# Performance work log

Hardware: AMD Instinct MI355X
Metric: run time of the kernel (lower is better)

## Reference

```python
import jax, jax.numpy as jnp
import numpy as np

B, S, DIM = 2, 1024, 4096
H, QLORA, KVLORA = 32, 1536, 512
NOPE, ROPE, VD = 128, 64, 128
QK_HEAD = NOPE + ROPE
SCALE = QK_HEAD ** -0.5
EPS = 1e-6
NEG = -1e9


def rms_norm(x, w):
    xf = x.astype(jnp.float32)
    y = xf * jax.lax.rsqrt(jnp.mean(xf * xf, axis=-1, keepdims=True) + EPS)
    return (y * w).astype(x.dtype)


def apply_rope(x, fc):
    # x: [b, s, h, r] with interleaved complex pairs; fc: [s, r//2, 2] = (cos, sin)
    b, s, h, r = x.shape
    xr = x.reshape(b, s, h, r // 2, 2)
    xe, xo = xr[..., 0], xr[..., 1]
    cos = fc[None, :, None, :, 0]
    sin = fc[None, :, None, :, 1]
    oe = xe * cos - xo * sin
    oo = xe * sin + xo * cos
    return jnp.stack([oe, oo], axis=-1).reshape(b, s, h, r)


def setup_inputs() -> dict:
    key = jax.random.key(0)
    ks = jax.random.split(key, 8)
    x = jax.random.normal(ks[0], (B, S, DIM), dtype=jnp.float32)
    pos = jnp.arange(S, dtype=jnp.float32)
    inv_freq = 1.0 / (10000.0 ** (jnp.arange(0, ROPE, 2, dtype=jnp.float32) / ROPE))
    ang = pos[:, None] * inv_freq[None, :]  # [S, ROPE//2]
    freqs_cis = jnp.stack([jnp.cos(ang), jnp.sin(ang)], axis=-1)  # [S, ROPE//2, 2]
    mask = jnp.triu(jnp.full((S, S), NEG, dtype=jnp.float32), k=1)
    def w(k, shape, fan_in):
        return jax.random.normal(k, shape, dtype=jnp.float32) * (fan_in ** -0.5)
    return {
        "x": x,
        "freqs_cis": freqs_cis,
        "mask": mask,
        "wq_a": w(ks[1], (DIM, QLORA), DIM),
        "q_norm_w": jnp.ones((QLORA,), jnp.float32),
        "wq_b": w(ks[2], (QLORA, H * QK_HEAD), QLORA),
        "wkv_a": w(ks[3], (DIM, KVLORA + ROPE), DIM),
        "kv_norm_w": jnp.ones((KVLORA,), jnp.float32),
        "wkv_b": w(ks[4], (H, NOPE + VD, KVLORA), KVLORA),
        "wo": w(ks[5], (H * VD, DIM), H * VD),
        "start_pos": 0,
    }


def reference(x, freqs_cis, mask, wq_a, q_norm_w, wq_b, wkv_a, kv_norm_w, wkv_b, wo, start_pos):
    bsz, seqlen, _ = x.shape
    # low-rank Q projection: wq_b(q_norm(wq_a(x)))
    q = rms_norm(x @ wq_a, q_norm_w) @ wq_b
    q = q.reshape(bsz, seqlen, H, QK_HEAD)
    q_nope, q_pe = q[..., :NOPE], q[..., NOPE:]
    q_pe = apply_rope(q_pe, freqs_cis)
    # compressed KV latent + shared rope key
    kv = x @ wkv_a
    c_kv, k_pe = kv[..., :KVLORA], kv[..., KVLORA:]
    k_pe = apply_rope(k_pe[:, :, None, :], freqs_cis)[:, :, 0, :]  # [b, t, ROPE]
    # weight absorption: q_nope @ wkv_b[:, :NOPE]  -> latent space
    q_abs = jnp.einsum('bshd,hdc->bshc', q_nope, wkv_b[:, :NOPE])  # [b,s,h,KVLORA]
    kv_n = rms_norm(c_kv, kv_norm_w)  # kv_cache[:bsz, :end_pos] (start_pos==0 prefill)
    scores = (jnp.einsum('bshc,btc->bsht', q_abs, kv_n)
              + jnp.einsum('bshr,btr->bsht', q_pe, k_pe)) * SCALE
    scores = scores + mask[None, :, None, :]
    probs = jax.nn.softmax(scores.astype(jnp.float32), axis=-1).astype(x.dtype)
    out = jnp.einsum('bsht,btc->bshc', probs, kv_n)
    out = jnp.einsum('bshc,hdc->bshd', out, wkv_b[:, -VD:])  # [b,s,h,VD]
    out = out.reshape(bsz, seqlen, H * VD) @ wo
    return out
```

## Files before the change

### kernel.cpp

```cpp
#include <hip/hip_runtime.h>
#include <stdint.h>

typedef unsigned short u16;
typedef uint32_t u32;
typedef short bf16x8 __attribute__((ext_vector_type(8)));
typedef float f32x4 __attribute__((ext_vector_type(4)));

#define DEV_INLINE __device__ __forceinline__

DEV_INLINE float b2f(u16 u) { union { u32 u; float f; } a; a.u = ((u32)u) << 16; return a.f; }
DEV_INLINE u16 f2b(float f) {
    union { float f; u32 u; } a; a.f = f;
    u32 u = a.u;
    u += 0x7fffu + ((u >> 16) & 1u);
    return (u16)(u >> 16);
}

typedef __attribute__((address_space(1))) u32 as1_u32;
typedef __attribute__((address_space(3))) u32 as3_u32;
DEV_INLINE void async16(void* lds, const void* g) {
    __builtin_amdgcn_global_load_lds((as1_u32*)g, (as3_u32*)lds, 16, 0, 0);
}

template <int MODE, bool CMASK = false, bool KCAP = false, bool SWZ = false>
__global__ __launch_bounds__(256) void gemm_bt(
    const u16* __restrict__ Ab, const u16* __restrict__ Bb, void* __restrict__ Cv,
    int K, long lda, long ldb, long ldc,
    long zA1, long zA2, long zB1, long zB2, long zC1, long zC2,
    float scale)
{
    __shared__ __align__(16) u16 As[2][128 * 32];
    __shared__ __align__(16) u16 Bs[2][128 * 32];

    int bx = blockIdx.x, by = blockIdx.y, bz = blockIdx.z;
    if (SWZ) {
        const int gx = gridDim.x, gy = gridDim.y;
        const int nwg = gx * gy * (int)gridDim.z;
        const int lin = bx + gx * (by + gy * bz);
        const int q = nwg >> 3, r = nwg & 7;
        const int xcd = lin & 7, idx = lin >> 3;
        const int wg = (xcd < r ? xcd * (q + 1) : r * (q + 1) + (xcd - r) * q) + idx;
        bx = wg % gx;
        const int t = wg / gx;
        by = t % gy;
        bz = t / gy;
    }

    const long row0 = (long)by * 128;
    const long col0 = (long)bx * 128;
    if (CMASK && col0 > row0) return;

    const long zb = bz >> 5, zh = bz & 31;
    const u16* A = Ab + zb * zA1 + zh * zA2;
    const u16* B = Bb + zb * zB1 + zh * zB2;

    const int tid = threadIdx.x;
    const int w = tid >> 6, l = tid & 63;
    const int quad = l >> 4, lrow = l & 15;
    const int wm = w & 1, wn = w >> 1;

    f32x4 acc[4][4];
#pragma unroll
    for (int mi = 0; mi < 4; mi++)
#pragma unroll
        for (int ni = 0; ni < 4; ni++) {
            f32x4 zv = {0.f, 0.f, 0.f, 0.f};
            acc[mi][ni] = zv;
        }

    const u16* gA = A + (row0 + w * 16 + (l >> 2)) * lda + (l & 3) * 8;
    const u16* gB = B + (col0 + w * 16 + (l >> 2)) * ldb + (l & 3) * 8;
    const int lofs = (w * 16) * 32;
    const long a64 = 64 * lda, b64 = 64 * ldb;

    int nk = K >> 5;
    if (KCAP) {
        const int nkc = (int)(row0 >> 5) + 4;
        nk = nk < nkc ? nk : nkc;
    }

    async16(&As[0][lofs], gA);
    async16(&As[0][lofs + 64 * 32], gA + a64);
    async16(&Bs[0][lofs], gB);
    async16(&Bs[0][lofs + 64 * 32], gB + b64);
    gA += 32;
    gB += 32;

    int cur = 0;
    for (int kt = 0; kt < nk; ++kt) {
        __syncthreads();
        if (kt + 1 < nk) {
            const int nxt = cur ^ 1;
            async16(&As[nxt][lofs], gA);
            async16(&As[nxt][lofs + 64 * 32], gA + a64);
            async16(&Bs[nxt][lofs], gB);
            async16(&Bs[nxt][lofs + 64 * 32], gB + b64);
            gA += 32;
            gB += 32;
        }
        bf16x8 af[4], bfr[4];
#pragma unroll
        for (int i = 0; i < 4; i++)
            af[i] = *(const bf16x8*)&As[cur][(wm * 64 + i * 16 + lrow) * 32 + quad * 8];
#pragma unroll
        for (int i = 0; i < 4; i++)
            bfr[i] = *(const bf16x8*)&Bs[cur][(wn * 64 + i * 16 + lrow) * 32 + quad * 8];
#pragma unroll
        for (int mi = 0; mi < 4; mi++)
#pragma unroll
            for (int ni = 0; ni < 4; ni++)
                acc[mi][ni] = __builtin_amdgcn_mfma_f32_16x16x32_bf16(af[mi], bfr[ni], acc[mi][ni], 0, 0, 0);
        cur ^= 1;
    }

    const long crow = row0 + wm * 64 + quad * 4;
    const long ccol = col0 + wn * 64 + lrow;
    float* Cf = (float*)Cv + zb * zC1 + zh * zC2;
    u16* Cb = (u16*)Cv + zb * zC1 + zh * zC2;
#pragma unroll
    for (int mi = 0; mi < 4; mi++)
#pragma unroll
        for (int rr = 0; rr < 4; rr++) {
            const long r = crow + mi * 16 + rr;
#pragma unroll
            for (int ni = 0; ni < 4; ni++) {
                const long c = ccol + ni * 16;
                const float v = acc[mi][ni][rr];
                if constexpr (MODE == 0) {
                    Cf[r * ldc + c] = v;
                } else if constexpr (MODE == 1) {
                    Cb[r * ldc + c] = f2b(v);
                } else {
                    const float mv = (c > r) ? -1e9f : 0.f;
                    Cb[r * ldc + c] = f2b(v * scale + mv);
                }
            }
        }
}

DEV_INLINE float ldval(const float* p) { return *p; }
DEV_INLINE float ldval(const u16* p) { return b2f(*p); }

template <typename SRC>
__global__ __launch_bounds__(256) void transpose_b16(
    const SRC* __restrict__ src, u16* __restrict__ dst,
    int R, int C, long ldS, long ldD, long zS, long zD)
{
    __shared__ float t[32][33];
    src += (long)blockIdx.z * zS;
    dst += (long)blockIdx.z * zD;
    const int tx = threadIdx.x & 31, ty = threadIdx.x >> 5;
    const long c0 = (long)blockIdx.x * 32, r0 = (long)blockIdx.y * 32;
#pragma unroll
    for (int i = 0; i < 4; i++) {
        long r = r0 + ty + i * 8, c = c0 + tx;
        if (r < R && c < C) t[ty + i * 8][tx] = ldval(&src[r * ldS + c]);
    }
    __syncthreads();
#pragma unroll
    for (int i = 0; i < 4; i++) {
        long c = c0 + ty + i * 8, r = r0 + tx;
        if (r < R && c < C) dst[c * ldD + r] = f2b(t[tx][ty + i * 8]);
    }
}

__global__ __launch_bounds__(256) void conv_b16(
    const float* __restrict__ src, u16* __restrict__ dst,
    int C, long ldS, long ldD, long zS, long zD)
{
    const long r = blockIdx.x;
    const float* s = src + (long)blockIdx.z * zS + r * ldS;
    u16* d = dst + (long)blockIdx.z * zD + r * ldD;
    for (int c = threadIdx.x; c < C; c += 256) d[c] = f2b(s[c]);
}

__global__ __launch_bounds__(256) void rmsnorm_b16(
    const float* __restrict__ X, const float* __restrict__ W, u16* __restrict__ Y,
    int C, long ldx, long ldy)
{
    const long r = blockIdx.x;
    const float* x = X + r * ldx;
    u16* y = Y + r * ldy;
    float ss = 0.f;
    for (int c = threadIdx.x; c < C; c += 256) { float v = x[c]; ss += v * v; }
    for (int off = 32; off; off >>= 1) ss += __shfl_down(ss, off);
    __shared__ float red[4];
    if ((threadIdx.x & 63) == 0) red[threadIdx.x >> 6] = ss;
    __syncthreads();
    const float tot = red[0] + red[1] + red[2] + red[3];
    const float inv = rsqrtf(tot / (float)C + 1e-6f);
    for (int c = threadIdx.x; c < C; c += 256) y[c] = f2b(x[c] * inv * W[c]);
}

__global__ __launch_bounds__(256) void rope_k_kernel(
    const float* __restrict__ kv, const float* __restrict__ fc, u16* __restrict__ kcat)
{
    const int idx = blockIdx.x * 256 + threadIdx.x;
    const int n = idx >> 5, i = idx & 31;
    const int s = n & 1023;
    const float e = kv[(long)n * 2176 + 2048 + 2 * i];
    const float o = kv[(long)n * 2176 + 2048 + 2 * i + 1];
    const float cs = fc[s * 64 + 2 * i], sn = fc[s * 64 + 2 * i + 1];
    kcat[(long)n * 576 + 512 + 2 * i] = f2b(e * cs - o * sn);
    kcat[(long)n * 576 + 512 + 2 * i + 1] = f2b(e * sn + o * cs);
}

__global__ __launch_bounds__(256) void rope_q_kernel(
    const u16* __restrict__ q, const float* __restrict__ fc, u16* __restrict__ qcat)
{
    const long idx = (long)blockIdx.x * 256 + threadIdx.x;
    const int i = (int)(idx & 31);
    const long nh = idx >> 5;
    const int h = (int)(nh & 31);
    const long n = nh >> 5;
    const int s = (int)(n & 1023);
    const float e = b2f(q[n * 6144 + h * 192 + 128 + 2 * i]);
    const float o = b2f(q[n * 6144 + h * 192 + 128 + 2 * i + 1]);
    const float cs = fc[s * 64 + 2 * i], sn = fc[s * 64 + 2 * i + 1];
    u16* dst = qcat + ((long)h * 2048 + n) * 576 + 512 + 2 * i;
    dst[0] = f2b(e * cs - o * sn);
    dst[1] = f2b(e * sn + o * cs);
}

__global__ __launch_bounds__(256) void softmax_rows(u16* __restrict__ P)
{
    const long base = (long)blockIdx.x * 1024;
    const int s = blockIdx.x & 1023;
    const int kcap = (s & ~127) + 128;
    const int tid = threadIdx.x;
    __shared__ float red[8];
    float vals[4];
    float m = -3.4e38f;
#pragma unroll
    for (int i = 0; i < 4; i++) {
        const int c = tid + i * 256;
        float v = (c < kcap) ? b2f(P[base + c]) : -3.4e38f;
        vals[i] = v;
        m = fmaxf(m, v);
    }
    for (int off = 32; off; off >>= 1) m = fmaxf(m, __shfl_down(m, off));
    if ((tid & 63) == 0) red[tid >> 6] = m;
    __syncthreads();
    const float m4 = fmaxf(fmaxf(red[0], red[1]), fmaxf(red[2], red[3]));
    float e[4];
    float sum = 0.f;
#pragma unroll
    for (int i = 0; i < 4; i++) {
        e[i] = exp2f((vals[i] - m4) * 1.44269504088896f);
        sum += e[i];
    }
    for (int off = 32; off; off >>= 1) sum += __shfl_down(sum, off);
    if ((tid & 63) == 0) red[4 + (tid >> 6)] = sum;
    __syncthreads();
    const float inv = 1.0f / (red[4] + red[5] + red[6] + red[7]);
#pragma unroll
    for (int i = 0; i < 4; i++) {
        const int c = tid + i * 256;
        if (c < kcap) P[base + c] = f2b(e[i] * inv);
    }
}

__global__ void sentinel_kernel(float* out, float v) { out[0] = v; }

extern "C" void kernel_launch(void* const* d_in, const int* in_sizes, int n_in,
                              void* d_out, int out_size, void* d_ws, size_t ws_size,
                              hipStream_t stream)
{
    const float* x = (const float*)d_in[0];
    const float* fc = (const float*)d_in[1];
    const float* wq_a = (const float*)d_in[3];
    const float* qnw = (const float*)d_in[4];
    const float* wq_b = (const float*)d_in[5];
    const float* wkva = (const float*)d_in[6];
    const float* kvnw = (const float*)d_in[7];
    const float* wkvb = (const float*)d_in[8];
    const float* wo = (const float*)d_in[9];
    float* out = (float*)d_out;

    const size_t NEED = 251920384ULL;
    if (ws_size < NEED) {
        sentinel_kernel<<<1, 1, 0, stream>>>(out, (float)ws_size);
        return;
    }
    char* ws = (char*)d_ws;
    u16* wkbv   = (u16*)(ws + 0);
    u16* wo_t   = (u16*)(ws + 4194304);
    u16* kvn_t  = (u16*)(ws + 37748736);
    u16* kcat   = (u16*)(ws + 39845888);
    u16* qcat   = (u16*)(ws + 42205184);
    u16* o1     = (u16*)(ws + 42205184);
    u16* scores = (u16*)(ws + 117702656);
    u16*   xb     = (u16*)(ws + 117702656);
    u16*   wqkv_t = (u16*)(ws + 134479872);
    u16*   wq_b_t = (u16*)(ws + 152305664);
    u16*   wkbn_t = (u16*)(ws + 171180032);
    float* qk_lat = (float*)(ws + 175374336);
    u16*   qn     = (u16*)(ws + 193200128);
    u16*   q      = (u16*)(ws + 199491584);
    u16*   o2     = (u16*)(ws + 117702656);

    const dim3 blk(256);
    const float SCALE = 0.0721687836487032f;

    transpose_b16<float><<<dim3(48, 128, 1), blk, 0, stream>>>(wq_a, wqkv_t, 4096, 1536, 1536, 4096, 0, 0);
    transpose_b16<float><<<dim3(18, 128, 1), blk, 0, stream>>>(wkva, wqkv_t + (long)1536 * 4096, 4096, 576, 576, 4096, 0, 0);
    transpose_b16<float><<<dim3(192, 48, 1), blk, 0, stream>>>(wq_b, wq_b_t, 1536, 6144, 6144, 1536, 0, 0);
    transpose_b16<float><<<dim3(16, 4, 32), blk, 0, stream>>>(wkvb, wkbn_t, 128, 512, 512, 128, 256 * 512, 512 * 128);
    conv_b16<<<dim3(128, 1, 32), blk, 0, stream>>>(wkvb + 128 * 512, wkbv, 512, 512, 512, 256 * 512, 128 * 512);
    transpose_b16<float><<<dim3(128, 128, 1), blk, 0, stream>>>(wo, wo_t, 4096, 4096, 4096, 4096, 0, 0);
    conv_b16<<<dim3(2048, 1, 1), blk, 0, stream>>>(x, xb, 4096, 4096, 4096, 0, 0);

    gemm_bt<0, false, false, true><<<dim3(17, 16, 1), blk, 0, stream>>>(
        xb, wqkv_t, qk_lat, 4096, 4096, 4096, 2176, 0, 0, 0, 0, 0, 0, 1.f);
    rmsnorm_b16<<<2048, blk, 0, stream>>>(qk_lat, qnw, qn, 1536, 2176, 1536);
    rmsnorm_b16<<<2048, blk, 0, stream>>>(qk_lat + 1536, kvnw, kcat, 512, 2176, 576);
    rope_k_kernel<<<256, blk, 0, stream>>>(qk_lat, fc, kcat);
    transpose_b16<u16><<<dim3(16, 32, 2), blk, 0, stream>>>(kcat, kvn_t, 1024, 512, 576, 1024,
                                                            (long)1024 * 576, (long)512 * 1024);
    gemm_bt<1, false, false, true><<<dim3(48, 16, 1), blk, 0, stream>>>(
        qn, wq_b_t, q, 1536, 1536, 1536, 6144, 0, 0, 0, 0, 0, 0, 1.f);
    gemm_bt<1><<<dim3(4, 16, 32), blk, 0, stream>>>(q, wkbn_t, qcat, 128, 6144, 128, 576,
                                                    0, 192, 0, (long)512 * 128, 0, (long)2048 * 576, 1.f);
    rope_q_kernel<<<8192, blk, 0, stream>>>(q, fc, qcat);
    gemm_bt<2, true, false, true><<<dim3(8, 8, 64), blk, 0, stream>>>(
        qcat, kcat, scores, 576, 576, 576, 1024,
        (long)1024 * 576, (long)2048 * 576, (long)1024 * 576, 0,
        (long)32 * 1048576, 1048576, SCALE);
    softmax_rows<<<65536, blk, 0, stream>>>(scores);
    gemm_bt<1, false, true, true><<<dim3(4, 8, 64), blk, 0, stream>>>(
        scores, kvn_t, o1, 1024, 1024, 1024, 512,
        (long)32 * 1048576, 1048576, (long)512 * 1024, 0,
        (long)1024 * 512, (long)2048 * 512, 1.f);
    gemm_bt<1><<<dim3(1, 16, 32), blk, 0, stream>>>(o1, wkbv, o2, 512, 512, 512, 4096,
                                                    0, (long)2048 * 512, 0, (long)128 * 512, 0, 128, 1.f);
    gemm_bt<0, false, false, true><<<dim3(32, 16, 1), blk, 0, stream>>>(
        o2, wo_t, out, 4096, 4096, 4096, 4096, 0, 0, 0, 0, 0, 0, 1.f);
    (void)in_sizes; (void)n_in; (void)out_size; (void)d_in;
}
```

Before: 750.6 us.

## Fuse exp into score GEMM epilogue and defer softmax normalization to PV GEMM

The score GEMM epilogue now writes exp2 of the scaled scores directly, with masked entries set to zero. The separate row-softmax pass that read and rewrote the whole score matrix is gone. In its place, a light kernel sums each causal row prefix and stores its reciprocal, and the PV GEMM epilogue multiplies by it. Max subtraction is dropped, so numerical safety now depends on score magnitudes staying in range. The XCD swizzle is also enabled on the q-absorption and output-projection GEMMs.

Result: faster. 712.9 us (-5.0%).

```diff
diff --git a/kernel.cpp b/kernel.cpp
--- a/kernel.cpp
+++ b/kernel.cpp
@@ -22,12 +22,12 @@
     __builtin_amdgcn_global_load_lds((as1_u32*)g, (as3_u32*)lds, 16, 0, 0);
 }
 
-template <int MODE, bool CMASK = false, bool KCAP = false, bool SWZ = false>
+template <int MODE, bool CMASK = false, bool KCAP = false, bool SWZ = false, bool RSC = false>
 __global__ __launch_bounds__(256) void gemm_bt(
     const u16* __restrict__ Ab, const u16* __restrict__ Bb, void* __restrict__ Cv,
     int K, long lda, long ldb, long ldc,
     long zA1, long zA2, long zB1, long zB2, long zC1, long zC2,
-    float scale)
+    float scale, const float* __restrict__ rowinv)
 {
     __shared__ __align__(16) u16 As[2][128 * 32];
     __shared__ __align__(16) u16 Bs[2][128 * 32];
@@ -117,11 +117,14 @@
     const long ccol = col0 + wn * 64 + lrow;
     float* Cf = (float*)Cv + zb * zC1 + zh * zC2;
     u16* Cb = (u16*)Cv + zb * zC1 + zh * zC2;
+    const float lse = scale * 1.44269504088896f;
 #pragma unroll
     for (int mi = 0; mi < 4; mi++)
 #pragma unroll
         for (int rr = 0; rr < 4; rr++) {
             const long r = crow + mi * 16 + rr;
+            float rs = 1.f;
+            if (RSC) rs = rowinv[(long)bz * 1024 + r];
 #pragma unroll
             for (int ni = 0; ni < 4; ni++) {
                 const long c = ccol + ni * 16;
@@ -129,10 +132,10 @@
                 if constexpr (MODE == 0) {
                     Cf[r * ldc + c] = v;
                 } else if constexpr (MODE == 1) {
-                    Cb[r * ldc + c] = f2b(v);
+                    Cb[r * ldc + c] = f2b(RSC ? v * rs : v);
                 } else {
-                    const float mv = (c > r) ? -1e9f : 0.f;
-                    Cb[r * ldc + c] = f2b(v * scale + mv);
+                    const float arg = (c > r) ? -1e30f : v * lse;
+                    Cb[r * ldc + c] = f2b(exp2f(arg));
                 }
             }
         }
@@ -222,42 +225,23 @@
     dst[1] = f2b(e * sn + o * cs);
 }
 
-__global__ __launch_bounds__(256) void softmax_rows(u16* __restrict__ P)
-{
-    const long base = (long)blockIdx.x * 1024;
-    const int s = blockIdx.x & 1023;
-    const int kcap = (s & ~127) + 128;
-    const int tid = threadIdx.x;
-    __shared__ float red[8];
-    float vals[4];
-    float m = -3.4e38f;
-#pragma unroll
-    for (int i = 0; i < 4; i++) {
-        const int c = tid + i * 256;
-        float v = (c < kcap) ? b2f(P[base + c]) : -3.4e38f;
-        vals[i] = v;
-        m = fmaxf(m, v);
-    }
-    for (int off = 32; off; off >>= 1) m = fmaxf(m, __shfl_down(m, off));
-    if ((tid & 63) == 0) red[tid >> 6] = m;
-    __syncthreads();
-    const float m4 = fmaxf(fmaxf(red[0], red[1]), fmaxf(red[2], red[3]));
-    float e[4];
-    float sum = 0.f;
-#pragma unroll
-    for (int i = 0; i < 4; i++) {
-        e[i] = exp2f((vals[i] - m4) * 1.44269504088896f);
-        sum += e[i];
-    }
-    for (int off = 32; off; off >>= 1) sum += __shfl_down(sum, off);
-    if ((tid & 63) == 0) red[4 + (tid >> 6)] = sum;
-    __syncthreads();
-    const float inv = 1.0f / (red[4] + red[5] + red[6] + red[7]);
-#pragma unroll
-    for (int i = 0; i < 4; i++) {
-        const int c = tid + i * 256;
-        if (c < kcap) P[base + c] = f2b(e[i] * inv);
-    }
+__global__ __launch_bounds__(256) void rowsum_inv(
+    const u16* __restrict__ P, float* __restrict__ inv)
+{
+    const int zt = blockIdx.y;
+    const int row0 = blockIdx.x * 128;
+    const int kcap = row0 + 128;
+    const int t = threadIdx.x;
+    const int r = t >> 1, half = t & 1;
+    const u16* p = P + (long)zt * 1048576 + (long)(row0 + r) * 1024;
+    float s = 0.f;
+    for (int c = half * 8; c < kcap; c += 16) {
+        bf16x8 v = *(const bf16x8*)&p[c];
+#pragma unroll
+        for (int j = 0; j < 8; j++) s += b2f((u16)v[j]);
+    }
+    s += __shfl_xor(s, 1);
+    if (!half) inv[(long)zt * 1024 + row0 + r] = 1.0f / s;
 }
 
 __global__ void sentinel_kernel(float* out, float v) { out[0] = v; }
@@ -277,7 +261,7 @@
     const float* wo = (const float*)d_in[9];
     float* out = (float*)d_out;
 
-    const size_t NEED = 251920384ULL;
+    const size_t NEED = 252182528ULL;
     if (ws_size < NEED) {
         sentinel_kernel<<<1, 1, 0, stream>>>(out, (float)ws_size);
         return;
@@ -298,6 +282,7 @@
     u16*   qn     = (u16*)(ws + 193200128);
     u16*   q      = (u16*)(ws + 199491584);
     u16*   o2     = (u16*)(ws + 117702656);
+    float* inv_g  = (float*)(ws + 251920384);
 
     const dim3 blk(256);
     const float SCALE = 0.0721687836487032f;
@@ -311,29 +296,31 @@
     conv_b16<<<dim3(2048, 1, 1), blk, 0, stream>>>(x, xb, 4096, 4096, 4096, 0, 0);
 
     gemm_bt<0, false, false, true><<<dim3(17, 16, 1), blk, 0, stream>>>(
-        xb, wqkv_t, qk_lat, 4096, 4096, 4096, 2176, 0, 0, 0, 0, 0, 0, 1.f);
+        xb, wqkv_t, qk_lat, 4096, 4096, 4096, 2176, 0, 0, 0, 0, 0, 0, 1.f, nullptr);
     rmsnorm_b16<<<2048, blk, 0, stream>>>(qk_lat, qnw, qn, 1536, 2176, 1536);
     rmsnorm_b16<<<2048, blk, 0, stream>>>(qk_lat + 1536, kvnw, kcat, 512, 2176, 576);
     rope_k_kernel<<<256, blk, 0, stream>>>(qk_lat, fc, kcat);
     transpose_b16<u16><<<dim3(16, 32, 2), blk, 0, stream>>>(kcat, kvn_t, 1024, 512, 576, 1024,
                                                             (long)1024 * 576, (long)512 * 1024);
     gemm_bt<1, false, false, true><<<dim3(48, 16, 1), blk, 0, stream>>>(
-        qn, wq_b_t, q, 1536, 1536, 1536, 6144, 0, 0, 0, 0, 0, 0, 1.f);
-    gemm_bt<1><<<dim3(4, 16, 32), blk, 0, stream>>>(q, wkbn_t, qcat, 128, 6144, 128, 576,
-                                                    0, 192, 0, (long)512 * 128, 0, (long)2048 * 576, 1.f);
+        qn, wq_b_t, q, 1536, 1536, 1536, 6144, 0, 0, 0, 0, 0, 0, 1.f, nullptr);
+    gemm_bt<1, false, false, true><<<dim3(4, 16, 32), blk, 0, stream>>>(
+        q, wkbn_t, qcat, 128, 6144, 128, 576,
+        0, 192, 0, (long)512 * 128, 0, (long)2048 * 576, 1.f, nullptr);
     rope_q_kernel<<<8192, blk, 0, stream>>>(q, fc, qcat);
     gemm_bt<2, true, false, true><<<dim3(8, 8, 64), blk, 0, stream>>>(
         qcat, kcat, scores, 576, 576, 576, 1024,
         (long)1024 * 576, (long)2048 * 576, (long)1024 * 576, 0,
-        (long)32 * 1048576, 1048576, SCALE);
-    softmax_rows<<<65536, blk, 0, stream>>>(scores);
-    gemm_bt<1, false, true, true><<<dim3(4, 8, 64), blk, 0, stream>>>(
+        (long)32 * 1048576, 1048576, SCALE, nullptr);
+    rowsum_inv<<<dim3(8, 64), blk, 0, stream>>>(scores, inv_g);
+    gemm_bt<1, false, true, true, true><<<dim3(4, 8, 64), blk, 0, stream>>>(
         scores, kvn_t, o1, 1024, 1024, 1024, 512,
         (long)32 * 1048576, 1048576, (long)512 * 1024, 0,
-        (long)1024 * 512, (long)2048 * 512, 1.f);
-    gemm_bt<1><<<dim3(1, 16, 32), blk, 0, stream>>>(o1, wkbv, o2, 512, 512, 512, 4096,
-                                                    0, (long)2048 * 512, 0, (long)128 * 512, 0, 128, 1.f);
+        (long)1024 * 512, (long)2048 * 512, 1.f, inv_g);
+    gemm_bt<1, false, false, true><<<dim3(1, 16, 32), blk, 0, stream>>>(
+        o1, wkbv, o2, 512, 512, 512, 4096,
+        0, (long)2048 * 512, 0, (long)128 * 512, 0, 128, 1.f, nullptr);
     gemm_bt<0, false, false, true><<<dim3(32, 16, 1), blk, 0, stream>>>(
-        o2, wo_t, out, 4096, 4096, 4096, 4096, 0, 0, 0, 0, 0, 0, 1.f);
+        o2, wo_t, out, 4096, 4096, 4096, 4096, 0, 0, 0, 0, 0, 0, 1.f, nullptr);
     (void)in_sizes; (void)n_in; (void)out_size; (void)d_in;
 }
```
